# Optimization experiments

Hardware: AMD Instinct MI355X
Metric: run time of the kernel (lower is better)

The kernel has to match this reference:

```python
import jax, jax.numpy as jnp
import numpy as np

DIM = 1024
HEADS = 16
HEAD_DIM = DIM // HEADS
WINDOW = 512
NEG = -1e9  # matches masked_fill(-1e9) semantics; excluded keys get ~0 weight


def setup_inputs() -> dict:
    key = jax.random.key(0)
    ks = jax.random.split(key, 9)
    s = 1.0 / np.sqrt(DIM)
    inp = {"x": jax.random.normal(ks[0], (2, 4096, DIM), dtype=jnp.float32)}
    for i, name in enumerate(["q", "k", "v", "o"]):
        inp[f"W{name}"] = jax.random.uniform(ks[1 + 2 * i], (DIM, DIM), jnp.float32, -s, s)
        inp[f"b{name}"] = jax.random.uniform(ks[2 + 2 * i], (DIM,), jnp.float32, -s, s)
    return inp


def _sliding_window_attn(x, Wq, bq, Wk, bk, Wv, bv, Wo, bo):
    B, S, D = x.shape
    H, hd, W = HEADS, HEAD_DIM, WINDOW
    nb = S // W  # number of query blocks

    def proj(Wp, bp):
        y = x @ Wp.T + bp                       # [B,S,D]
        return y.reshape(B, S, H, hd).transpose(0, 2, 1, 3)  # [B,H,S,hd]

    q = proj(Wq, bq)
    k = proj(Wk, bk)
    v = proj(Wv, bv)

    scale = hd ** -0.5
    qb = q.reshape(B, H, nb, W, hd)

    def window_kv(t):
        # each query block n attends to blocks n-1 and n (2W keys)
        pad = jnp.concatenate([jnp.zeros((B, H, W, hd), t.dtype), t], axis=2)
        prev = pad[:, :, :S].reshape(B, H, nb, W, hd)
        cur = t.reshape(B, H, nb, W, hd)
        return jnp.concatenate([prev, cur], axis=3)  # [B,H,nb,2W,hd]

    kw = window_kv(k)
    vw = window_kv(v)

    scores = jnp.einsum('bhnqd,bhnkd->bhnqk', qb, kw) * scale  # [B,H,nb,W,2W]

    # key abs pos = n*W - W + t ; query abs pos = n*W + s
    t = jnp.arange(2 * W)            # [2W]
    s_ = jnp.arange(W)[:, None]      # [W,1]
    n = jnp.arange(nb)[:, None, None]  # [nb,1,1]
    valid = (t <= s_ + W) & (t >= s_ + 1) & (n * W - W + t >= 0)  # [nb,W,2W]
    scores = jnp.where(valid, scores, NEG)

    attn = jax.nn.softmax(scores, axis=-1)
    out = jnp.einsum('bhnqk,bhnkd->bhnqd', attn, vw)  # [B,H,nb,W,hd]
    out = out.reshape(B, H, S, hd).transpose(0, 2, 1, 3).reshape(B, S, D)
    return out @ Wo.T + bo


def reference(x, Wq, bq, Wk, bk, Wv, bv, Wo, bo):
    return _sliding_window_attn(x, Wq, bq, Wk, bk, Wv, bv, Wo, bo)
```

## Files before the change

kernel.cpp:

```cpp
#include <hip/hip_runtime.h>
#include <hip/hip_bf16.h>

typedef __bf16 bf16_t;
typedef __attribute__((ext_vector_type(8))) __bf16 bfrag;
typedef __attribute__((ext_vector_type(4))) __bf16 bf16x4;
typedef __attribute__((ext_vector_type(4))) float f32x4;

#define SEQ    4096
#define NDIM   1024
#define NHEAD  16
#define HD     64
#define NBATCH 2
#define MROWS  (NBATCH * SEQ)
#define LQK    2048
#define PSTR   76

__device__ __forceinline__ void gload_lds16(const bf16_t* g, bf16_t* l) {
    __builtin_amdgcn_global_load_lds(
        (const __attribute__((address_space(1))) unsigned int*)g,
        (__attribute__((address_space(3))) unsigned int*)l,
        16, 0, 0);
}

#define BAR()  do { asm volatile("" ::: "memory"); __builtin_amdgcn_s_barrier(); \
                    asm volatile("" ::: "memory"); } while (0)
#define LGKM0() do { asm volatile("s_waitcnt lgkmcnt(0)" ::: "memory"); \
                     __builtin_amdgcn_sched_barrier(0); } while (0)
#define VMC(n)  asm volatile("s_waitcnt vmcnt(" #n ")" ::: "memory")

__global__ __launch_bounds__(512, 2)
void gemm256(const bf16_t* __restrict__ A, int lda,
             const bf16_t* __restrict__ W,
             const float* __restrict__ b0p, const float* __restrict__ b1p,
             const float* __restrict__ b2p, float qscale,
             bf16_t* __restrict__ C, int ldc, int K,
             bf16_t* __restrict__ VtOut)
{
    extern __shared__ bf16_t LDS[];

    const int tid  = threadIdx.x;
    const int lane = tid & 63;
    const int n16  = lane & 15;
    const int quad = lane >> 4;
    const int wid  = tid >> 6;
    const int wm   = wid >> 2;
    const int wn   = wid & 3;
    const int row0 = blockIdx.y * 256;
    const int col0 = blockIdx.x * 256;
    const int NT   = K >> 6;

    int poff0 = tid * 16;
    int loff0 = poff0 ^ (((poff0 >> 9) & 1) << 5);
    int poff1 = 8192 + tid * 16;
    int loff1 = poff1 ^ (((poff1 >> 9) & 1) << 5);
    const int r0 = loff0 >> 6, c0 = (loff0 & 63) >> 1;
    const int r1 = loff1 >> 6, c1 = (loff1 & 63) >> 1;
    const bf16_t* Asrc0 = A + (size_t)(row0 + r0) * lda + c0;
    const bf16_t* Asrc1 = A + (size_t)(row0 + r1) * lda + c1;
    const bf16_t* Wsrc0 = W + (size_t)(col0 + r0) * K + c0;
    const bf16_t* Wsrc1 = W + (size_t)(col0 + r1) * K + c1;
    bf16_t* const dst0 = LDS;
    const int wb = wid * 512;

    f32x4 acc[8][4];
#pragma unroll
    for (int m = 0; m < 8; m++)
#pragma unroll
        for (int j = 0; j < 4; j++) acc[m][j] = (f32x4){0.f, 0.f, 0.f, 0.f};

#define SLOT(d, op, h) ((d) * 32768 + (op) * 16384 + (h) * 8192)
#define STAGE(srcA0, srcA1, slot, gk)                                   \
    do { gload_lds16((srcA0) + (gk), dst0 + (slot) + wb);               \
         gload_lds16((srcA1) + (gk), dst0 + (slot) + 4096 + wb); } while (0)

    STAGE(Wsrc0, Wsrc1, SLOT(0,1,0), 0);
    STAGE(Asrc0, Asrc1, SLOT(0,0,0), 0);
    STAGE(Wsrc0, Wsrc1, SLOT(0,1,1), 32);
    STAGE(Asrc0, Asrc1, SLOT(0,0,1), 32);
    STAGE(Wsrc0, Wsrc1, SLOT(1,1,0), 64);
    STAGE(Asrc0, Asrc1, SLOT(1,0,0), 64);
    STAGE(Wsrc0, Wsrc1, SLOT(1,1,1), 96);
    VMC(10);
    BAR();

    for (int s = 0; s < NT; ++s) {
        const int d = s & 1;
        bfrag af[4], bf[4];

        {
            const bf16_t* sA = LDS + SLOT(d, 0, 0);
            const bf16_t* sB = LDS + SLOT(d, 1, 0);
#pragma unroll
            for (int f = 0; f < 4; f++) {
                int off = ((wm * 128 + f * 16 + n16) << 6) + (quad << 4);
                off ^= ((off >> 9) & 1) << 5;
                af[f] = *(const bfrag*)((const char*)sA + off);
            }
#pragma unroll
            for (int j = 0; j < 4; j++) {
                int off = ((wn * 64 + j * 16 + n16) << 6) + (quad << 4);
                off ^= ((off >> 9) & 1) << 5;
                bf[j] = *(const bfrag*)((const char*)sB + off);
            }
        }
        if (s + 1 < NT) STAGE(Asrc0, Asrc1, SLOT(d ^ 1, 0, 1), (s + 1) * 64 + 32);
        BAR();
        LGKM0();
        __builtin_amdgcn_s_setprio(1);
#pragma unroll
        for (int f = 0; f < 4; f++)
#pragma unroll
            for (int j = 0; j < 4; j++)
                acc[f][j] = __builtin_amdgcn_mfma_f32_16x16x32_bf16(af[f], bf[j], acc[f][j], 0, 0, 0);
        __builtin_amdgcn_s_setprio(0);
        BAR();

        {
            const bf16_t* sA = LDS + SLOT(d, 0, 0);
#pragma unroll
            for (int f = 0; f < 4; f++) {
                int off = ((wm * 128 + (f + 4) * 16 + n16) << 6) + (quad << 4);
                off ^= ((off >> 9) & 1) << 5;
                af[f] = *(const bfrag*)((const char*)sA + off);
            }
        }
        if (s + 2 < NT) STAGE(Wsrc0, Wsrc1, SLOT(d, 1, 0), (s + 2) * 64);
        BAR();
        LGKM0();
        __builtin_amdgcn_s_setprio(1);
#pragma unroll
        for (int f = 0; f < 4; f++)
#pragma unroll
            for (int j = 0; j < 4; j++)
                acc[f + 4][j] = __builtin_amdgcn_mfma_f32_16x16x32_bf16(af[f], bf[j], acc[f + 4][j], 0, 0, 0);
        __builtin_amdgcn_s_setprio(0);
        if (s < NT - 2)       VMC(10);
        else if (s == NT - 2) VMC(8);
        else                  VMC(0);
        BAR();

        {
            const bf16_t* sA = LDS + SLOT(d, 0, 1);
            const bf16_t* sB = LDS + SLOT(d, 1, 1);
#pragma unroll
            for (int f = 0; f < 4; f++) {
                int off = ((wm * 128 + f * 16 + n16) << 6) + (quad << 4);
                off ^= ((off >> 9) & 1) << 5;
                af[f] = *(const bfrag*)((const char*)sA + off);
            }
#pragma unroll
            for (int j = 0; j < 4; j++) {
                int off = ((wn * 64 + j * 16 + n16) << 6) + (quad << 4);
                off ^= ((off >> 9) & 1) << 5;
                bf[j] = *(const bfrag*)((const char*)sB + off);
            }
        }
        if (s + 2 < NT) STAGE(Asrc0, Asrc1, SLOT(d, 0, 0), (s + 2) * 64);
        BAR();
        LGKM0();
        __builtin_amdgcn_s_setprio(1);
#pragma unroll
        for (int f = 0; f < 4; f++)
#pragma unroll
            for (int j = 0; j < 4; j++)
                acc[f][j] = __builtin_amdgcn_mfma_f32_16x16x32_bf16(af[f], bf[j], acc[f][j], 0, 0, 0);
        __builtin_amdgcn_s_setprio(0);
        BAR();

        {
            const bf16_t* sA = LDS + SLOT(d, 0, 1);
#pragma unroll
            for (int f = 0; f < 4; f++) {
                int off = ((wm * 128 + (f + 4) * 16 + n16) << 6) + (quad << 4);
                off ^= ((off >> 9) & 1) << 5;
                af[f] = *(const bfrag*)((const char*)sA + off);
            }
        }
        if (s + 2 < NT) STAGE(Wsrc0, Wsrc1, SLOT(d, 1, 1), (s + 2) * 64 + 32);
        BAR();
        LGKM0();
        __builtin_amdgcn_s_setprio(1);
#pragma unroll
        for (int f = 0; f < 4; f++)
#pragma unroll
            for (int j = 0; j < 4; j++)
                acc[f + 4][j] = __builtin_amdgcn_mfma_f32_16x16x32_bf16(af[f], bf[j], acc[f + 4][j], 0, 0, 0);
        __builtin_amdgcn_s_setprio(0);
        if (s + 1 < NT) {
            if (s < NT - 2) VMC(10);
            else            VMC(4);
        }
        BAR();
    }
#undef STAGE
#undef SLOT

    const float* bias = (col0 < 1024) ? b0p : (col0 < 2048 ? b1p : b2p);
    const float bsc   = (col0 < 1024) ? qscale : 1.0f;
    const int bcol0   = col0 & 1023;

    if (col0 < 2048 || VtOut == nullptr) {
#pragma unroll
        for (int m = 0; m < 8; m++)
#pragma unroll
            for (int j = 0; j < 4; j++)
#pragma unroll
                for (int r = 0; r < 4; r++) {
                    int row = row0 + wm * 128 + m * 16 + quad * 4 + r;
                    int col = wn * 64 + j * 16 + n16;
                    float v = acc[m][j][r] + bias[bcol0 + col] * bsc;
                    C[(size_t)row * ldc + col0 + col] = (bf16_t)v;
                }
    } else {
#pragma unroll
        for (int m = 0; m < 8; m++) {
#pragma unroll
            for (int j = 0; j < 4; j++) {
                int dg     = col0 + wn * 64 + j * 16 + n16 - 2048;
                int token0 = row0 + wm * 128 + m * 16 + quad * 4;
                int bb     = token0 >> 12;
                float bv   = bias[bcol0 + wn * 64 + j * 16 + n16];
                size_t vrow = ((size_t)bb * NHEAD + (dg >> 6)) * HD + (dg & 63);
                bf16x4 pk;
#pragma unroll
                for (int r = 0; r < 4; r++) pk[r] = (__bf16)(acc[m][j][r] + bv);
                *(bf16x4*)&VtOut[vrow * SEQ + (token0 & (SEQ - 1))] = pk;
            }
        }
    }
}

template <typename OT>
__global__ __launch_bounds__(256, 2)
void gemm_bt(const bf16_t* __restrict__ A, int lda,
             const bf16_t* __restrict__ W,
             const float* __restrict__ b0p, const float* __restrict__ b1p,
             const float* __restrict__ b2p, float qscale,
             OT* __restrict__ C, int ldc, int K,
             bf16_t* __restrict__ VtOut)
{
    __shared__ __align__(16) bf16_t As[128 * 32];
    __shared__ __align__(16) bf16_t Bs[128 * 32];

    const int tid  = threadIdx.x;
    const int lane = tid & 63;
    const int wid  = tid >> 6;
    const int n16  = lane & 15;
    const int quad = lane >> 4;
    const int row0 = blockIdx.y * 128;
    const int col0 = blockIdx.x * 128;
    const int wrow = (wid >> 1) * 64;
    const int wcol = (wid & 1) * 64;
    const float* bias = (col0 < 1024) ? b0p : (col0 < 2048 ? b1p : b2p);
    const float bsc = (col0 < 1024) ? qscale : 1.0f;
    const int bcol0 = col0 & 1023;

    f32x4 acc[4][4];
#pragma unroll
    for (int i = 0; i < 4; i++)
#pragma unroll
        for (int j = 0; j < 4; j++) acc[i][j] = (f32x4){0.f, 0.f, 0.f, 0.f};

    for (int k0 = 0; k0 < K; k0 += 32) {
#pragma unroll
        for (int it = 0; it < 2; it++) {
            int idx = tid + it * 256;
            int r   = idx >> 2;
            int c   = (idx & 3) * 8;
            gload_lds16(A + (size_t)(row0 + r) * lda + k0 + c, &As[(it * 256 + wid * 64) * 8]);
            gload_lds16(W + (size_t)(col0 + r) * K   + k0 + c, &Bs[(it * 256 + wid * 64) * 8]);
        }
        __syncthreads();

        bfrag af[4], bfg[4];
#pragma unroll
        for (int i = 0; i < 4; i++)
            af[i] = *(const bfrag*)(&As[(wrow + i * 16 + n16) * 32 + quad * 8]);
#pragma unroll
        for (int j = 0; j < 4; j++)
            bfg[j] = *(const bfrag*)(&Bs[(wcol + j * 16 + n16) * 32 + quad * 8]);

#pragma unroll
        for (int i = 0; i < 4; i++)
#pragma unroll
            for (int j = 0; j < 4; j++)
                acc[i][j] = __builtin_amdgcn_mfma_f32_16x16x32_bf16(af[i], bfg[j], acc[i][j], 0, 0, 0);
        __syncthreads();
    }

    if (col0 < 2048 || VtOut == nullptr) {
#pragma unroll
        for (int i = 0; i < 4; i++)
#pragma unroll
            for (int j = 0; j < 4; j++)
#pragma unroll
                for (int r = 0; r < 4; r++) {
                    int row = row0 + wrow + i * 16 + quad * 4 + r;
                    int col = wcol + j * 16 + n16;
                    float v = acc[i][j][r] + bias[bcol0 + col] * bsc;
                    C[(size_t)row * ldc + col0 + col] = (OT)v;
                }
    } else {
#pragma unroll
        for (int i = 0; i < 4; i++) {
#pragma unroll
            for (int j = 0; j < 4; j++) {
                int dg     = col0 + wcol + j * 16 + n16 - 2048;
                int token0 = row0 + wrow + i * 16 + quad * 4;
                int bb     = token0 >> 12;
                float bv   = bias[bcol0 + wcol + j * 16 + n16];
                size_t vrow = ((size_t)bb * NHEAD + (dg >> 6)) * HD + (dg & 63);
                bf16x4 pk;
#pragma unroll
                for (int r = 0; r < 4; r++) pk[r] = (__bf16)(acc[i][j][r] + bv);
                *(bf16x4*)&VtOut[vrow * SEQ + (token0 & (SEQ - 1))] = pk;
            }
        }
    }
}

__global__ __launch_bounds__(256)
void cast_x(const float* __restrict__ s, bf16_t* __restrict__ d)
{
    size_t i = ((size_t)blockIdx.x * 256 + threadIdx.x) * 8;
    float4 a = *(const float4*)(s + i);
    float4 b = *(const float4*)(s + i + 4);
    bfrag o;
    o[0] = (__bf16)a.x; o[1] = (__bf16)a.y; o[2] = (__bf16)a.z; o[3] = (__bf16)a.w;
    o[4] = (__bf16)b.x; o[5] = (__bf16)b.y; o[6] = (__bf16)b.z; o[7] = (__bf16)b.w;
    *(bfrag*)(d + i) = o;
}

__global__ __launch_bounds__(256)
void cast_w(const float* __restrict__ wq, const float* __restrict__ wk,
            const float* __restrict__ wv, const float* __restrict__ wo,
            bf16_t* __restrict__ d)
{
    size_t t   = (size_t)blockIdx.x * 256 + threadIdx.x;
    int    sel = (int)(t >> 17);
    const float* s = sel == 0 ? wq : (sel == 1 ? wk : (sel == 2 ? wv : wo));
    const float sc = (sel == 0) ? 0.125f : 1.0f;
    size_t off = (t & 131071) * 8;
    float4 a = *(const float4*)(s + off);
    float4 b = *(const float4*)(s + off + 4);
    bfrag o;
    o[0] = (__bf16)(a.x * sc); o[1] = (__bf16)(a.y * sc);
    o[2] = (__bf16)(a.z * sc); o[3] = (__bf16)(a.w * sc);
    o[4] = (__bf16)(b.x * sc); o[5] = (__bf16)(b.y * sc);
    o[6] = (__bf16)(b.z * sc); o[7] = (__bf16)(b.w * sc);
    *(bfrag*)(d + (size_t)sel * 1048576 + off) = o;
}

__global__ __launch_bounds__(256, 4)
void attn_win(const bf16_t* __restrict__ QK, const bf16_t* __restrict__ Vt,
              bf16_t* __restrict__ AO)
{
    __shared__ __align__(16) bf16_t Ks[2][64 * 72];
    __shared__ __align__(16) bf16_t Pw[4][32 * PSTR];

    const int tid  = threadIdx.x;
    const int wid  = tid >> 6;
    const int lane = tid & 63;
    const int n16  = lane & 15;
    const int quad = lane >> 4;

    const int lin = blockIdx.x;
    const int sub = lin >> 3;
    const int bh  = (lin & 7) * 4 + (sub >> 5);
    const int qt  = sub & 31;
    const int qb0 = qt * 128;

    const int b  = bh >> 4, h = bh & 15;
    const size_t bS   = (size_t)b * SEQ;
    const size_t hoff = (size_t)h * HD;
    const bf16_t* Vb  = Vt + (size_t)bh * HD * SEQ;
    const int wstart  = qb0 - 512;
    const int it0     = (qb0 < 512) ? ((512 - qb0) >> 6) : 0;

    const int srow  = tid >> 2;
    const int scol0 = (tid & 3) * 16;

    const int qwmin = qb0 + wid * 32;
    const int qwmax = qwmin + 31;
    int qa[2];
    bfrag bq0[2], bq1[2];
#pragma unroll
    for (int qg = 0; qg < 2; qg++) {
        qa[qg] = qwmin + qg * 16 + n16;
        bq0[qg] = *(const bfrag*)(&QK[(bS + qa[qg]) * LQK + hoff + quad * 8]);
        bq1[qg] = *(const bfrag*)(&QK[(bS + qa[qg]) * LQK + hoff + 32 + quad * 8]);
    }

    f32x4 ao[2][4];
#pragma unroll
    for (int qg = 0; qg < 2; qg++)
#pragma unroll
        for (int j = 0; j < 4; j++) ao[qg][j] = (f32x4){0.f, 0.f, 0.f, 0.f};
    float m[2] = {-1e30f, -1e30f}, l[2] = {0.f, 0.f};

    uint4 kp0, kp1;
    {
        const bf16_t* src = &QK[(bS + wstart + it0 * 64 + srow) * LQK + 1024 + hoff + scol0];
        kp0 = *(const uint4*)(src);
        kp1 = *(const uint4*)(src + 8);
    }

    for (int it = it0; it < 10; ++it) {
        const int k0 = wstart + it * 64;
        const int pb = it & 1;
        *(uint4*)(&Ks[pb][srow * 72 + scol0])     = kp0;
        *(uint4*)(&Ks[pb][srow * 72 + scol0 + 8]) = kp1;
        __syncthreads();
        if (it < 9) {
            const bf16_t* src = &QK[(bS + wstart + (it + 1) * 64 + srow) * LQK + 1024 + hoff + scol0];
            kp0 = *(const uint4*)(src);
            kp1 = *(const uint4*)(src + 8);
        }

        if (k0 > qwmax || k0 + 63 < qwmin - 511) continue;

        f32x4 a[2][4];
#pragma unroll
        for (int nt = 0; nt < 4; nt++) {
            bfrag ak0 = *(const bfrag*)(&Ks[pb][(nt * 16 + n16) * 72 + quad * 8]);
            bfrag ak1 = *(const bfrag*)(&Ks[pb][(nt * 16 + n16) * 72 + 32 + quad * 8]);
#pragma unroll
            for (int qg = 0; qg < 2; qg++) {
                f32x4 s4 = (f32x4){0.f, 0.f, 0.f, 0.f};
                s4 = __builtin_amdgcn_mfma_f32_16x16x32_bf16(ak0, bq0[qg], s4, 0, 0, 0);
                s4 = __builtin_amdgcn_mfma_f32_16x16x32_bf16(ak1, bq1[qg], s4, 0, 0, 0);
                a[qg][nt] = s4;
            }
        }

#pragma unroll
        for (int qg = 0; qg < 2; qg++) {
            const int gmin = qwmin + qg * 16, gmax = gmin + 15;
            const bool msk = !((k0 >= gmax - 511) & (k0 + 63 <= gmin));
            if (msk) {
#pragma unroll
                for (int nt = 0; nt < 4; nt++)
#pragma unroll
                    for (int r = 0; r < 4; r++) {
                        int ka = k0 + nt * 16 + quad * 4 + r;
                        bool valid = (ka >= qa[qg] - 511) & (ka <= qa[qg]);
                        if (!valid) a[qg][nt][r] = -1e30f;
                    }
            }

            float cm = -1e30f;
#pragma unroll
            for (int nt = 0; nt < 4; nt++)
#pragma unroll
                for (int r = 0; r < 4; r++) cm = fmaxf(cm, a[qg][nt][r]);
            cm = fmaxf(cm, __shfl_xor(cm, 16, 64));
            cm = fmaxf(cm, __shfl_xor(cm, 32, 64));
            float mn    = fmaxf(m[qg], cm);
            float alpha = __expf(m[qg] - mn);
            m[qg] = mn;
#pragma unroll
            for (int j = 0; j < 4; j++)
#pragma unroll
                for (int r = 0; r < 4; r++) ao[qg][j][r] *= alpha;

            float lacc = 0.f;
#pragma unroll
            for (int nt = 0; nt < 4; nt++) {
                bf16x4 pk;
#pragma unroll
                for (int r = 0; r < 4; r++) {
                    float p = __expf(a[qg][nt][r] - m[qg]);
                    lacc += p;
                    pk[r] = (__bf16)p;
                }
                *(bf16x4*)&Pw[wid][(qg * 16 + n16) * PSTR + nt * 16 + quad * 4] = pk;
            }
            l[qg] = l[qg] * alpha + lacc;
        }

#pragma unroll
        for (int ks = 0; ks < 2; ks++) {
            bfrag bp[2];
#pragma unroll
            for (int qg = 0; qg < 2; qg++)
                bp[qg] = *(const bfrag*)(&Pw[wid][(qg * 16 + n16) * PSTR + ks * 32 + quad * 8]);
#pragma unroll
            for (int j = 0; j < 4; j++) {
                bfrag av = *(const bfrag*)(&Vb[(size_t)(j * 16 + n16) * SEQ
                                               + k0 + ks * 32 + quad * 8]);
#pragma unroll
                for (int qg = 0; qg < 2; qg++)
                    ao[qg][j] = __builtin_amdgcn_mfma_f32_16x16x32_bf16(av, bp[qg], ao[qg][j], 0, 0, 0);
            }
        }
    }

#pragma unroll
    for (int qg = 0; qg < 2; qg++) {
        float lv = l[qg];
        lv += __shfl_xor(lv, 16, 64);
        lv += __shfl_xor(lv, 32, 64);
        const float inv = 1.0f / lv;
#pragma unroll
        for (int j = 0; j < 4; j++) {
            bf16x4 pk;
#pragma unroll
            for (int r = 0; r < 4; r++) pk[r] = (__bf16)(ao[qg][j][r] * inv);
            *(bf16x4*)&AO[(bS + qa[qg]) * NDIM + hoff + j * 16 + quad * 4] = pk;
        }
    }
}

extern "C" void kernel_launch(void* const* d_in, const int* in_sizes, int n_in,
                              void* d_out, int out_size, void* d_ws, size_t ws_size,
                              hipStream_t stream)
{
    const float* x  = (const float*)d_in[0];
    const float* Wq = (const float*)d_in[1];
    const float* bq = (const float*)d_in[2];
    const float* Wk = (const float*)d_in[3];
    const float* bk = (const float*)d_in[4];
    const float* Wv = (const float*)d_in[5];
    const float* bv = (const float*)d_in[6];
    const float* Wo = (const float*)d_in[7];
    const float* bo = (const float*)d_in[8];
    float* out = (float*)d_out;

    const size_t QK_E = (size_t)MROWS * LQK;
    const size_t X_E  = (size_t)MROWS * NDIM;
    if (ws_size < (QK_E + X_E + 4u * 1048576u) * sizeof(bf16_t)) return;

    bf16_t* QKb = (bf16_t*)d_ws;
    bf16_t* AbX = QKb + QK_E;
    bf16_t* Wc  = AbX + X_E;
    bf16_t* Wob = Wc + 3u * 1048576u;
    bf16_t* Vtg = (bf16_t*)d_out;

    static int lds_ok = -1;
    if (lds_ok < 0)
        lds_ok = (hipFuncSetAttribute((const void*)gemm256,
                   hipFuncAttributeMaxDynamicSharedMemorySize, 131072) == hipSuccess) ? 1 : 0;

    dim3 blk(256);

    cast_x<<<dim3(4096), blk, 0, stream>>>(x, AbX);
    cast_w<<<dim3(2048), blk, 0, stream>>>(Wq, Wk, Wv, Wo, Wc);

    if (lds_ok) {
        gemm256<<<dim3(3072 / 256, MROWS / 256), dim3(512), 131072, stream>>>(
            AbX, NDIM, Wc, bq, bk, bv, 0.125f, QKb, LQK, NDIM, Vtg);
    } else {
        gemm_bt<bf16_t><<<dim3(3072 / 128, MROWS / 128), blk, 0, stream>>>(
            AbX, NDIM, Wc, bq, bk, bv, 0.125f, QKb, LQK, NDIM, Vtg);
    }

    attn_win<<<dim3(1024), dim3(256), 0, stream>>>(QKb, Vtg, AbX);

    gemm_bt<float><<<dim3(NDIM / 128, MROWS / 128), blk, 0, stream>>>(
        AbX, NDIM, Wob, bo, bo, bo, 1.0f, out, NDIM, NDIM, nullptr);
}
```

Baseline: 274.4 us.

## Prefetch LDS fragments one phase ahead to overlap reads with MFMA

Restructures the GEMM main loop so LDS fragment reads for the next MFMA phase are issued before the current phase's MFMAs, using separate register buffers (aL0/aH0/aL1/aH1/b0f/b1f). The explicit lgkmcnt(0) waits are removed, letting the compiler place waits. The vmcnt thresholds are tightened to match the earlier consumption. This hides LDS read latency behind matrix math, at the cost of more VGPRs under a 512-thread, 2-block launch bound.

After: 275.9 us. No clear change (+0.5%).

```diff
diff --git a/kernel.cpp b/kernel.cpp
--- a/kernel.cpp
+++ b/kernel.cpp
@@ -24,8 +24,6 @@
 
 #define BAR()  do { asm volatile("" ::: "memory"); __builtin_amdgcn_s_barrier(); \
                     asm volatile("" ::: "memory"); } while (0)
-#define LGKM0() do { asm volatile("s_waitcnt lgkmcnt(0)" ::: "memory"); \
-                     __builtin_amdgcn_sched_barrier(0); } while (0)
 #define VMC(n)  asm volatile("s_waitcnt vmcnt(" #n ")" ::: "memory")
 
 __global__ __launch_bounds__(512, 2)
@@ -72,6 +70,15 @@
 #define STAGE(srcA0, srcA1, slot, gk)                                   \
     do { gload_lds16((srcA0) + (gk), dst0 + (slot) + wb);               \
          gload_lds16((srcA1) + (gk), dst0 + (slot) + 4096 + wb); } while (0)
+#define RD4(dst, slot, rbase)                                           \
+    do { _Pragma("unroll")                                              \
+        for (int f = 0; f < 4; f++) {                                   \
+            int off = (((rbase) + f * 16 + n16) << 6) + (quad << 4);    \
+            off ^= ((off >> 9) & 1) << 5;                               \
+            dst[f] = *(const bfrag*)((const char*)(LDS + (slot)) + off);\
+        } } while (0)
+
+    bfrag aL0[4], aH0[4], aL1[4], aH1[4], b0f[4], b1f[4];
 
     STAGE(Wsrc0, Wsrc1, SLOT(0,1,0), 0);
     STAGE(Asrc0, Asrc1, SLOT(0,0,0), 0);
@@ -80,120 +87,74 @@
     STAGE(Wsrc0, Wsrc1, SLOT(1,1,0), 64);
     STAGE(Asrc0, Asrc1, SLOT(1,0,0), 64);
     STAGE(Wsrc0, Wsrc1, SLOT(1,1,1), 96);
-    VMC(10);
+    VMC(6);
     BAR();
+    RD4(aL0, SLOT(0,0,0), wm * 128);
+    RD4(b0f, SLOT(0,1,0), wn * 64);
 
     for (int s = 0; s < NT; ++s) {
         const int d = s & 1;
-        bfrag af[4], bf[4];
-
-        {
-            const bf16_t* sA = LDS + SLOT(d, 0, 0);
-            const bf16_t* sB = LDS + SLOT(d, 1, 0);
-#pragma unroll
-            for (int f = 0; f < 4; f++) {
-                int off = ((wm * 128 + f * 16 + n16) << 6) + (quad << 4);
-                off ^= ((off >> 9) & 1) << 5;
-                af[f] = *(const bfrag*)((const char*)sA + off);
-            }
-#pragma unroll
-            for (int j = 0; j < 4; j++) {
-                int off = ((wn * 64 + j * 16 + n16) << 6) + (quad << 4);
-                off ^= ((off >> 9) & 1) << 5;
-                bf[j] = *(const bfrag*)((const char*)sB + off);
-            }
-        }
+
+        RD4(aH0, SLOT(d, 0, 0), wm * 128 + 64);
         if (s + 1 < NT) STAGE(Asrc0, Asrc1, SLOT(d ^ 1, 0, 1), (s + 1) * 64 + 32);
         BAR();
-        LGKM0();
         __builtin_amdgcn_s_setprio(1);
 #pragma unroll
         for (int f = 0; f < 4; f++)
 #pragma unroll
             for (int j = 0; j < 4; j++)
-                acc[f][j] = __builtin_amdgcn_mfma_f32_16x16x32_bf16(af[f], bf[j], acc[f][j], 0, 0, 0);
+                acc[f][j] = __builtin_amdgcn_mfma_f32_16x16x32_bf16(aL0[f], b0f[j], acc[f][j], 0, 0, 0);
         __builtin_amdgcn_s_setprio(0);
         BAR();
 
-        {
-            const bf16_t* sA = LDS + SLOT(d, 0, 0);
-#pragma unroll
-            for (int f = 0; f < 4; f++) {
-                int off = ((wm * 128 + (f + 4) * 16 + n16) << 6) + (quad << 4);
-                off ^= ((off >> 9) & 1) << 5;
-                af[f] = *(const bfrag*)((const char*)sA + off);
-            }
-        }
+        RD4(aL1, SLOT(d, 0, 1), wm * 128);
+        RD4(b1f, SLOT(d, 1, 1), wn * 64);
         if (s + 2 < NT) STAGE(Wsrc0, Wsrc1, SLOT(d, 1, 0), (s + 2) * 64);
         BAR();
-        LGKM0();
         __builtin_amdgcn_s_setprio(1);
 #pragma unroll
         for (int f = 0; f < 4; f++)
 #pragma unroll
             for (int j = 0; j < 4; j++)
-                acc[f + 4][j] = __builtin_amdgcn_mfma_f32_16x16x32_bf16(af[f], bf[j], acc[f + 4][j], 0, 0, 0);
+                acc[f + 4][j] = __builtin_amdgcn_mfma_f32_16x16x32_bf16(aH0[f], b0f[j], acc[f + 4][j], 0, 0, 0);
         __builtin_amdgcn_s_setprio(0);
-        if (s < NT - 2)       VMC(10);
-        else if (s == NT - 2) VMC(8);
+        if (s < NT - 2)       VMC(6);
+        else if (s == NT - 2) VMC(4);
         else                  VMC(0);
         BAR();
 
-        {
-            const bf16_t* sA = LDS + SLOT(d, 0, 1);
-            const bf16_t* sB = LDS + SLOT(d, 1, 1);
-#pragma unroll
-            for (int f = 0; f < 4; f++) {
-                int off = ((wm * 128 + f * 16 + n16) << 6) + (quad << 4);
-                off ^= ((off >> 9) & 1) << 5;
-                af[f] = *(const bfrag*)((const char*)sA + off);
-            }
-#pragma unroll
-            for (int j = 0; j < 4; j++) {
-                int off = ((wn * 64 + j * 16 + n16) << 6) + (quad << 4);
-                off ^= ((off >> 9) & 1) << 5;
-                bf[j] = *(const bfrag*)((const char*)sB + off);
-            }
-        }
+        RD4(aH1, SLOT(d, 0, 1), wm * 128 + 64);
         if (s + 2 < NT) STAGE(Asrc0, Asrc1, SLOT(d, 0, 0), (s + 2) * 64);
         BAR();
-        LGKM0();
         __builtin_amdgcn_s_setprio(1);
 #pragma unroll
         for (int f = 0; f < 4; f++)
 #pragma unroll
             for (int j = 0; j < 4; j++)
-                acc[f][j] = __builtin_amdgcn_mfma_f32_16x16x32_bf16(af[f], bf[j], acc[f][j], 0, 0, 0);
+                acc[f][j] = __builtin_amdgcn_mfma_f32_16x16x32_bf16(aL1[f], b1f[j], acc[f][j], 0, 0, 0);
         __builtin_amdgcn_s_setprio(0);
         BAR();
 
-        {
-            const bf16_t* sA = LDS + SLOT(d, 0, 1);
-#pragma unroll
-            for (int f = 0; f < 4; f++) {
-                int off = ((wm * 128 + (f + 4) * 16 + n16) << 6) + (quad << 4);
-                off ^= ((off >> 9) & 1) << 5;
-                af[f] = *(const bfrag*)((const char*)sA + off);
-            }
+        if (s + 1 < NT) {
+            RD4(aL0, SLOT(d ^ 1, 0, 0), wm * 128);
+            RD4(b0f, SLOT(d ^ 1, 1, 0), wn * 64);
         }
         if (s + 2 < NT) STAGE(Wsrc0, Wsrc1, SLOT(d, 1, 1), (s + 2) * 64 + 32);
         BAR();
-        LGKM0();
         __builtin_amdgcn_s_setprio(1);
 #pragma unroll
         for (int f = 0; f < 4; f++)
 #pragma unroll
             for (int j = 0; j < 4; j++)
-                acc[f + 4][j] = __builtin_amdgcn_mfma_f32_16x16x32_bf16(af[f], bf[j], acc[f + 4][j], 0, 0, 0);
+                acc[f + 4][j] = __builtin_amdgcn_mfma_f32_16x16x32_bf16(aH1[f], b1f[j], acc[f + 4][j], 0, 0, 0);
         __builtin_amdgcn_s_setprio(0);
-        if (s + 1 < NT) {
-            if (s < NT - 2) VMC(10);
-            else            VMC(4);
-        }
+        if (s < NT - 2)       VMC(6);
+        else if (s == NT - 2) VMC(0);
         BAR();
     }
 #undef STAGE
 #undef SLOT
+#undef RD4
 
     const float* bias = (col0 < 1024) ? b0p : (col0 < 2048 ? b1p : b2p);
     const float bsc   = (col0 < 1024) ? qscale : 1.0f;
```
